# Kernel tuning notes

Measured on AMD Instinct MI355X. Metric: run time of the kernel, lower is better.

## Reference

```python
import jax, jax.numpy as jnp
import numpy as np

N = 100000          # nodes
E = 1600000         # edges (avg degree 16)
IN_F = 256          # in_features
OUT_F = 128         # out_features


def setup_inputs() -> dict:
    key = jax.random.key(0)
    k1, k2, k3, k4, k5 = jax.random.split(key, 5)
    x = jax.random.normal(k1, (N, IN_F), dtype=jnp.float32)
    edge_index = jax.random.randint(k2, (2, E), 0, N, dtype=jnp.int32)
    # xavier_uniform-style init (gain 1.414)
    def xav(k, shape):
        fan_in, fan_out = shape[0], shape[1]
        bound = 1.414 * np.sqrt(6.0 / (fan_in + fan_out))
        return jax.random.uniform(k, shape, jnp.float32, -bound, bound)
    W = xav(k3, (IN_F, OUT_F))
    a = xav(k4, (2 * OUT_F, 1))
    W_em = xav(k5, (IN_F, OUT_F))
    return {"x": x, "edge_index": edge_index, "W": W, "a": a, "W_em": W_em}


def reference(x, edge_index, W, a, W_em):
    # DisGALayer.forward_sparse, att_type=1, gnn_type='AT', eval mode (dropout off)
    src = edge_index[0]
    dst = edge_index[1]
    h = x @ W                                   # [N, OUT_F]
    # edge_e = cat(h[src], h[dst]) @ a  ==  h[src]@a_src + h[dst]@a_dst
    a_src, a_dst = a[:OUT_F], a[OUT_F:]
    edge_e = h[src] @ a_src + h[dst] @ a_dst    # [E, 1]
    edge_ob = jax.nn.sigmoid(edge_e)            # [E, 1]
    # sp_softmax: softmax of edge values grouped by row (src)
    v = jnp.exp(edge_ob - jax.lax.stop_gradient(edge_ob.max()))
    denom = jax.ops.segment_sum(v, src, num_segments=N)   # [N, 1]
    attention = v / denom[src]                  # [E, 1]
    # sp_matmul: h_prime[i] = sum_{e: src(e)=i} att_e * h_em[dst(e)]
    h_em = x @ W_em                             # [N, OUT_F]
    h_prime = jax.ops.segment_sum(attention * h_em[dst], src, num_segments=N)
    return h_prime, edge_e
```

## Files before the change

### kernel.cpp

```cpp
#include <hip/hip_runtime.h>
#include <hip/hip_bf16.h>

#define NN 100000
#define NE 1600000
#define INF 256
#define OUTF 128
#define NBK ((NN + 127) / 128)
#define CHUNK 4096
#define NBA ((NE + CHUNK - 1) / CHUNK)
#define NGRP (NN / 32)
#define SCAP 6144

typedef __attribute__((ext_vector_type(8))) short short8;
typedef __attribute__((ext_vector_type(4))) float f32x4;

static __device__ __forceinline__ short f2bf(float f) {
    __hip_bfloat16 h = __float2bfloat16(f);
    return *reinterpret_cast<short*>(&h);
}

__global__ void k_setup(const float* __restrict__ W, const float* __restrict__ a,
                        const float* __restrict__ Wem, const int* __restrict__ src,
                        float* __restrict__ wsv, float* __restrict__ wdv,
                        ushort* __restrict__ Bsw, int* __restrict__ cntA) {
    const int b = blockIdx.x, t = threadIdx.x;
    if (b == 0) {
        const float* Wr = W + (size_t)t * OUTF;
        float sa = 0.f, sb = 0.f;
        #pragma unroll 8
        for (int k = 0; k < OUTF; ++k) {
            float w = Wr[k];
            sa += w * a[k];
            sb += w * a[OUTF + k];
        }
        wsv[t] = sa;
        wdv[t] = sb;
    } else if (b <= 8) {
        const int kt = b - 1;
        for (int idx = t; idx < 4096; idx += 256) {
            const int ct = idx >> 9;
            const int lane = (idx >> 3) & 63;
            const int j = idx & 7;
            const int k = kt * 32 + (lane >> 4) * 8 + j;
            const int c = ct * 16 + (lane & 15);
            Bsw[((size_t)(kt * 8 + ct) * 64 + lane) * 8 + j] =
                (ushort)f2bf(Wem[(size_t)k * OUTF + c]);
        }
    } else {
        __shared__ int cnt[NBK];
        const int c = b - 9;
        const int e0 = c * CHUNK;
        for (int i = t; i < NBK; i += 256) cnt[i] = 0;
        __syncthreads();
        for (int i = t; i < CHUNK; i += 256) {
            const int e = e0 + i;
            if (e < NE) atomicAdd(&cnt[src[e] >> 7], 1);
        }
        __syncthreads();
        for (int i = t; i < NBK; i += 256) cntA[(size_t)c * NBK + i] = cnt[i];
    }
}

__global__ __launch_bounds__(512) void k_mmcs(
    const float* __restrict__ x, const ushort* __restrict__ Bsw,
    const float* __restrict__ wsv, const float* __restrict__ wdv,
    const int* __restrict__ cntA,
    float* __restrict__ s1, float* __restrict__ s2,
    char* __restrict__ hem8, float* __restrict__ scaleA,
    int* __restrict__ baseA, int* __restrict__ bsumB) {
    __shared__ int sm[512];
    const int b = blockIdx.x;
    const int t = threadIdx.x;
    if (b < 782) {
        const int w = t >> 6, lane = t & 63;
        const int br = b * 128 + w * 16;
        const int r0 = lane & 15, kq = lane >> 4;
        const int row = br + r0;
        const int rowc = (row < NN) ? row : NN - 1;
        const float* xp = x + (size_t)rowc * INF + kq * 8;
        const short8* bp = reinterpret_cast<const short8*>(Bsw);

        f32x4 acc[8];
        #pragma unroll
        for (int ct = 0; ct < 8; ++ct) acc[ct] = (f32x4){0.f, 0.f, 0.f, 0.f};
        float sa = 0.f, sb = 0.f;

        #pragma unroll
        for (int kt = 0; kt < 8; ++kt) {
            const float4 a0 = *reinterpret_cast<const float4*>(xp + kt * 32);
            const float4 a1 = *reinterpret_cast<const float4*>(xp + kt * 32 + 4);
            const float4 w0 = *reinterpret_cast<const float4*>(wsv + kt * 32 + kq * 8);
            const float4 w1 = *reinterpret_cast<const float4*>(wsv + kt * 32 + kq * 8 + 4);
            const float4 u0 = *reinterpret_cast<const float4*>(wdv + kt * 32 + kq * 8);
            const float4 u1 = *reinterpret_cast<const float4*>(wdv + kt * 32 + kq * 8 + 4);
            sa += a0.x * w0.x + a0.y * w0.y + a0.z * w0.z + a0.w * w0.w
                + a1.x * w1.x + a1.y * w1.y + a1.z * w1.z + a1.w * w1.w;
            sb += a0.x * u0.x + a0.y * u0.y + a0.z * u0.z + a0.w * u0.w
                + a1.x * u1.x + a1.y * u1.y + a1.z * u1.z + a1.w * u1.w;
            short8 af;
            af[0] = f2bf(a0.x); af[1] = f2bf(a0.y); af[2] = f2bf(a0.z); af[3] = f2bf(a0.w);
            af[4] = f2bf(a1.x); af[5] = f2bf(a1.y); af[6] = f2bf(a1.z); af[7] = f2bf(a1.w);
            #pragma unroll
            for (int ct = 0; ct < 8; ++ct) {
                const short8 bf = bp[(size_t)(kt * 8 + ct) * 64 + lane];
                acc[ct] = __builtin_amdgcn_mfma_f32_16x16x32_bf16(af, bf, acc[ct], 0, 0, 0);
            }
        }

        sa += __shfl_xor(sa, 16); sa += __shfl_xor(sa, 32);
        sb += __shfl_xor(sb, 16); sb += __shfl_xor(sb, 32);
        if (kq == 0 && row < NN) { s1[row] = sa; s2[row] = sb; }

        float mx[4];
        #pragma unroll
        for (int i = 0; i < 4; ++i) {
            float m = 0.f;
            #pragma unroll
            for (int ct = 0; ct < 8; ++ct) m = fmaxf(m, fabsf(acc[ct][i]));
            m = fmaxf(m, __shfl_xor(m, 1));
            m = fmaxf(m, __shfl_xor(m, 2));
            m = fmaxf(m, __shfl_xor(m, 4));
            m = fmaxf(m, __shfl_xor(m, 8));
            mx[i] = m;
        }
        #pragma unroll
        for (int i = 0; i < 4; ++i) {
            const int rr = br + kq * 4 + i;
            if (rr < NN) {
                if (r0 == 0) scaleA[rr] = mx[i];
                const float inv = (mx[i] > 0.f) ? 127.f / mx[i] : 0.f;
                #pragma unroll
                for (int ct = 0; ct < 8; ++ct) {
                    int q = (int)rintf(acc[ct][i] * inv);
                    q = (q > 127) ? 127 : ((q < -127) ? -127 : q);
                    hem8[((size_t)(ct >> 1) * NN + rr) * 32 + (ct & 1) * 16 + r0] =
                        (char)q;
                }
            }
        }
    } else {
        const int bb = b - 782;
        const int v = (t < NBA) ? cntA[(size_t)t * NBK + bb] : 0;
        sm[t] = v;
        __syncthreads();
        for (int off = 1; off < 512; off <<= 1) {
            const int add = (t >= off) ? sm[t - off] : 0;
            __syncthreads();
            sm[t] += add;
            __syncthreads();
        }
        if (t < NBA) baseA[(size_t)t * NBK + bb] = sm[t] - v;
        if (t == 511) bsumB[bb] = sm[511];
    }
}

__global__ __launch_bounds__(1024) void k_bbase(
    const int* __restrict__ bsumB, int* __restrict__ bbase,
    int* __restrict__ offs) {
    __shared__ int sm[1024];
    const int t = threadIdx.x;
    const int v = (t < NBK) ? bsumB[t] : 0;
    sm[t] = v;
    __syncthreads();
    for (int off = 1; off < 1024; off <<= 1) {
        const int add = (t >= off) ? sm[t - off] : 0;
        __syncthreads();
        sm[t] += add;
        __syncthreads();
    }
    if (t < NBK) bbase[t] = sm[t] - v;
    if (t == 0) { bbase[NBK] = NE; offs[NN] = NE; }
}

__global__ __launch_bounds__(256) void k_binA(
    const int* __restrict__ src, const int* __restrict__ dst,
    const float* __restrict__ s1, const float* __restrict__ s2,
    float* __restrict__ ee_out, const int* __restrict__ bbase,
    const int* __restrict__ baseA, int2* __restrict__ ebA) {
    __shared__ int base[NBK];
    __shared__ int cnt[NBK];
    const int t = threadIdx.x;
    const int c = blockIdx.x;
    const int e0 = c * CHUNK;
    for (int i = t; i < NBK; i += 256) {
        base[i] = bbase[i] + baseA[(size_t)c * NBK + i];
        cnt[i] = 0;
    }
    __syncthreads();
    for (int i = t; i < CHUNK; i += 256) {
        const int e = e0 + i;
        if (e < NE) {
            const int s = src[e], d = dst[e];
            const float ee = s1[s] + s2[d];
            __builtin_nontemporal_store(ee, ee_out + e);
            const float ob = 1.f / (1.f + __expf(-ee));
            const float v = __expf(ob);
            int vq = (int)((v - 1.f) * 16384.f + 0.5f);
            vq = (vq > 32767) ? 32767 : vq;
            const int bk = s >> 7;
            const int r = atomicAdd(&cnt[bk], 1);
            ebA[base[bk] + r] = make_int2((d << 7) | (s & 127), vq);
        }
    }
}

__global__ __launch_bounds__(256) void k_sortB(
    const int* __restrict__ bbase, const int2* __restrict__ ebA,
    const float* __restrict__ scaleA,
    uint* __restrict__ ebB, int* __restrict__ offs) {
    __shared__ uint rx[SCAP];
    __shared__ ushort ry[SCAP];
    __shared__ int cnt[128];
    __shared__ int sum[128];
    __shared__ int sm[128];
    __shared__ int cur[128];
    __shared__ float fsl[128];
    const int b = blockIdx.x, t = threadIdx.x;
    const int n0 = b << 7;
    const int lo = bbase[b];
    const int hi = bbase[b + 1];
    const int n = hi - lo;
    if (t < 128) { cnt[t] = 0; sum[t] = 0; }
    __syncthreads();
    for (int i = t; i < n; i += 256) {
        const int2 r = ebA[lo + i];
        if (i < SCAP) { rx[i] = (uint)r.x; ry[i] = (ushort)r.y; }
        const int sidx = r.x & 127;
        atomicAdd(&cnt[sidx], 1);
        atomicAdd(&sum[sidx], r.y);
    }
    __syncthreads();
    const int v = (t < 128) ? cnt[t] : 0;
    if (t < 128) sm[t] = v;
    __syncthreads();
    for (int off = 1; off < 128; off <<= 1) {
        int add = 0;
        if (t < 128 && t >= off) add = sm[t - off];
        __syncthreads();
        if (t < 128) sm[t] += add;
        __syncthreads();
    }
    if (t < 128) {
        const int excl = sm[t] - v;
        cur[t] = excl;
        const int node = n0 + t;
        if (node < NN) offs[node] = lo + excl;
        fsl[t] = (v > 0) ? 1.f / (float)(v * 16384 + sum[t]) : 0.f;
    }
    __syncthreads();
    for (int i = t; i < n; i += 256) {
        uint x;
        int y;
        if (i < SCAP) { x = rx[i]; y = (int)ry[i]; }
        else { const int2 r = ebA[lo + i]; x = (uint)r.x; y = r.y; }
        const int sidx = x & 127;
        const uint d = x >> 7;
        const float att = (float)(16384 + y) * fsl[sidx];
        const float w = att * scaleA[d];
        int wq = (int)(w * 1024.f + 0.5f);
        wq = (wq > 32767) ? 32767 : wq;
        const int p = atomicAdd(&cur[sidx], 1);
        ebB[lo + p] = (d << 15) | (uint)wq;
    }
}

__global__ __launch_bounds__(256) void k_aggregate(
    const uint* __restrict__ eb, const int* __restrict__ offs,
    const char* __restrict__ hem8, float* __restrict__ out0) {
    const int slice = blockIdx.x & 3;
    const int grp = blockIdx.x >> 2;
    const int t = threadIdx.x;
    const int node = grp * 32 + (t >> 3);
    const int f = t & 7;
    const char* base = hem8 + (size_t)slice * NN * 32 + f * 4;
    const int beg = offs[node];
    const int end = offs[node + 1];

    int a0 = 0, a1 = 0, a2 = 0, a3 = 0;
    int j = beg;
    for (; j + 4 <= end; j += 4) {
        const uint r0 = eb[j];
        const uint r1 = eb[j + 1];
        const uint r2 = eb[j + 2];
        const uint r3 = eb[j + 3];
        const int w0 = (int)(r0 & 0x7fffu);
        const int w1 = (int)(r1 & 0x7fffu);
        const int w2 = (int)(r2 & 0x7fffu);
        const int w3 = (int)(r3 & 0x7fffu);
        const uint u0 = *reinterpret_cast<const uint*>(base + ((size_t)(r0 >> 15)) * 32);
        const uint u1 = *reinterpret_cast<const uint*>(base + ((size_t)(r1 >> 15)) * 32);
        const uint u2 = *reinterpret_cast<const uint*>(base + ((size_t)(r2 >> 15)) * 32);
        const uint u3 = *reinterpret_cast<const uint*>(base + ((size_t)(r3 >> 15)) * 32);
        a0 += w0 * (((int)(u0 << 24)) >> 24) + w1 * (((int)(u1 << 24)) >> 24)
            + w2 * (((int)(u2 << 24)) >> 24) + w3 * (((int)(u3 << 24)) >> 24);
        a1 += w0 * (((int)(u0 << 16)) >> 24) + w1 * (((int)(u1 << 16)) >> 24)
            + w2 * (((int)(u2 << 16)) >> 24) + w3 * (((int)(u3 << 16)) >> 24);
        a2 += w0 * (((int)(u0 << 8)) >> 24) + w1 * (((int)(u1 << 8)) >> 24)
            + w2 * (((int)(u2 << 8)) >> 24) + w3 * (((int)(u3 << 8)) >> 24);
        a3 += w0 * (((int)u0) >> 24) + w1 * (((int)u1) >> 24)
            + w2 * (((int)u2) >> 24) + w3 * (((int)u3) >> 24);
    }
    for (; j < end; ++j) {
        const uint r0 = eb[j];
        const int w0 = (int)(r0 & 0x7fffu);
        const uint u0 = *reinterpret_cast<const uint*>(base + ((size_t)(r0 >> 15)) * 32);
        a0 += w0 * (((int)(u0 << 24)) >> 24);
        a1 += w0 * (((int)(u0 << 16)) >> 24);
        a2 += w0 * (((int)(u0 << 8)) >> 24);
        a3 += w0 * (((int)u0) >> 24);
    }
    const float s = 1.f / (1024.f * 127.f);
    f32x4 o = {a0 * s, a1 * s, a2 * s, a3 * s};
    *reinterpret_cast<f32x4*>(
        out0 + (size_t)node * OUTF + slice * 32 + f * 4) = o;
}

extern "C" void kernel_launch(void* const* d_in, const int* in_sizes, int n_in,
                              void* d_out, int out_size, void* d_ws, size_t ws_size,
                              hipStream_t stream) {
    const float* x   = (const float*)d_in[0];
    const int* eidx  = (const int*)d_in[1];
    const float* W   = (const float*)d_in[2];
    const float* a   = (const float*)d_in[3];
    const float* Wem = (const float*)d_in[4];

    const int* src = eidx;
    const int* dst = eidx + NE;

    float* out0 = (float*)d_out;
    float* out1 = out0 + (size_t)NN * OUTF;

    float* wsv    = (float*)d_ws;
    float* wdv    = wsv + 256;
    float* s1     = wdv + 256;
    float* s2     = s1 + NN;
    float* scaleA = s2 + NN;
    ushort* Bsw   = (ushort*)(scaleA + NN);
    int* offs     = (int*)(Bsw + 32768);
    int* bsumB    = offs + NN + 4;
    int* bbase    = bsumB + 784;
    int* cntA     = bbase + 788;
    int* baseA    = cntA + NBA * NBK;
    int2* ebA     = (int2*)(baseA + NBA * NBK);
    uint* ebB     = (uint*)(ebA + NE);
    char* hem8    = (char*)(ebB + NE);

    hipLaunchKernelGGL(k_setup, dim3(9 + NBA), dim3(256), 0, stream,
                       W, a, Wem, src, wsv, wdv, Bsw, cntA);
    hipLaunchKernelGGL(k_mmcs, dim3(782 + 782), dim3(512), 0, stream,
                       x, Bsw, wsv, wdv, cntA, s1, s2, hem8, scaleA,
                       baseA, bsumB);
    hipLaunchKernelGGL(k_bbase, dim3(1), dim3(1024), 0, stream, bsumB, bbase, offs);
    hipLaunchKernelGGL(k_binA, dim3(NBA), dim3(256), 0, stream,
                       src, dst, s1, s2, out1, bbase, baseA, ebA);
    hipLaunchKernelGGL(k_sortB, dim3(NBK), dim3(256), 0, stream,
                       bbase, ebA, scaleA, ebB, offs);
    hipLaunchKernelGGL(k_aggregate, dim3(4 * NGRP), dim3(256), 0, stream,
                       ebB, offs, hem8, out0);
}
```

Before: 156.1 us.

## Shrink mmcs blocks, prefetch x rows, and pack int8 stores via shuffles

The fused matmul/scan kernel now uses 256-thread blocks covering 64 rows each, doubling the matmul grid, and the scan half processes two elements per thread. All x loads for a row are issued up front into registers before the MFMA loop, so global memory latency overlaps. The int8 quantized output is packed across lanes with shuffles so one thread writes a 4-byte word instead of four single-byte stores. This raises register pressure and adds shuffle instructions in exchange for fewer, wider stores and more loads in flight.

```diff
diff --git a/kernel.cpp b/kernel.cpp
--- a/kernel.cpp
+++ b/kernel.cpp
@@ -10,6 +10,7 @@
 #define NBA ((NE + CHUNK - 1) / CHUNK)
 #define NGRP (NN / 32)
 #define SCAP 6144
+#define NMM 1563
 
 typedef __attribute__((ext_vector_type(8))) short short8;
 typedef __attribute__((ext_vector_type(4))) float f32x4;
@@ -61,7 +62,7 @@
     }
 }
 
-__global__ __launch_bounds__(512) void k_mmcs(
+__global__ __launch_bounds__(256) void k_mmcs(
     const float* __restrict__ x, const ushort* __restrict__ Bsw,
     const float* __restrict__ wsv, const float* __restrict__ wdv,
     const int* __restrict__ cntA,
@@ -71,15 +72,22 @@
     __shared__ int sm[512];
     const int b = blockIdx.x;
     const int t = threadIdx.x;
-    if (b < 782) {
+    if (b < NMM) {
         const int w = t >> 6, lane = t & 63;
-        const int br = b * 128 + w * 16;
+        const int br = b * 64 + w * 16;
         const int r0 = lane & 15, kq = lane >> 4;
         const int row = br + r0;
         const int rowc = (row < NN) ? row : NN - 1;
         const float* xp = x + (size_t)rowc * INF + kq * 8;
+
+        float4 xa[16];
+        #pragma unroll
+        for (int kt = 0; kt < 8; ++kt) {
+            xa[2 * kt]     = *reinterpret_cast<const float4*>(xp + kt * 32);
+            xa[2 * kt + 1] = *reinterpret_cast<const float4*>(xp + kt * 32 + 4);
+        }
+
         const short8* bp = reinterpret_cast<const short8*>(Bsw);
-
         f32x4 acc[8];
         #pragma unroll
         for (int ct = 0; ct < 8; ++ct) acc[ct] = (f32x4){0.f, 0.f, 0.f, 0.f};
@@ -87,8 +95,8 @@
 
         #pragma unroll
         for (int kt = 0; kt < 8; ++kt) {
-            const float4 a0 = *reinterpret_cast<const float4*>(xp + kt * 32);
-            const float4 a1 = *reinterpret_cast<const float4*>(xp + kt * 32 + 4);
+            const float4 a0 = xa[2 * kt];
+            const float4 a1 = xa[2 * kt + 1];
             const float4 w0 = *reinterpret_cast<const float4*>(wsv + kt * 32 + kq * 8);
             const float4 w1 = *reinterpret_cast<const float4*>(wsv + kt * 32 + kq * 8 + 4);
             const float4 u0 = *reinterpret_cast<const float4*>(wdv + kt * 32 + kq * 8);
@@ -126,31 +134,41 @@
         #pragma unroll
         for (int i = 0; i < 4; ++i) {
             const int rr = br + kq * 4 + i;
-            if (rr < NN) {
-                if (r0 == 0) scaleA[rr] = mx[i];
-                const float inv = (mx[i] > 0.f) ? 127.f / mx[i] : 0.f;
-                #pragma unroll
-                for (int ct = 0; ct < 8; ++ct) {
-                    int q = (int)rintf(acc[ct][i] * inv);
-                    q = (q > 127) ? 127 : ((q < -127) ? -127 : q);
-                    hem8[((size_t)(ct >> 1) * NN + rr) * 32 + (ct & 1) * 16 + r0] =
-                        (char)q;
+            const float inv = (mx[i] > 0.f) ? 127.f / mx[i] : 0.f;
+            if (r0 == 0 && rr < NN) scaleA[rr] = mx[i];
+            #pragma unroll
+            for (int ct = 0; ct < 8; ++ct) {
+                int q = (int)rintf(acc[ct][i] * inv);
+                q = (q > 127) ? 127 : ((q < -127) ? -127 : q);
+                uint p = (uint)(q & 255);
+                p |= ((uint)__shfl_xor((int)p, 1) & 255u) << 8;
+                uint word = p | ((uint)__shfl_xor((int)p, 2) << 16);
+                if ((r0 & 3) == 0 && rr < NN) {
+                    *reinterpret_cast<uint*>(
+                        hem8 + ((size_t)(ct >> 1) * NN + rr) * 32
+                             + (ct & 1) * 16 + r0) = word;
                 }
             }
         }
     } else {
-        const int bb = b - 782;
-        const int v = (t < NBA) ? cntA[(size_t)t * NBK + bb] : 0;
-        sm[t] = v;
+        const int bb = b - NMM;
+        const int v0 = (t < NBA) ? cntA[(size_t)t * NBK + bb] : 0;
+        const int t2 = t + 256;
+        const int v1 = (t2 < NBA) ? cntA[(size_t)t2 * NBK + bb] : 0;
+        sm[t] = v0;
+        sm[t2] = v1;
         __syncthreads();
         for (int off = 1; off < 512; off <<= 1) {
-            const int add = (t >= off) ? sm[t - off] : 0;
+            const int a0 = (t >= off) ? sm[t - off] : 0;
+            const int a1 = (t2 >= off) ? sm[t2 - off] : 0;
             __syncthreads();
-            sm[t] += add;
+            sm[t] += a0;
+            sm[t2] += a1;
             __syncthreads();
         }
-        if (t < NBA) baseA[(size_t)t * NBK + bb] = sm[t] - v;
-        if (t == 511) bsumB[bb] = sm[511];
+        if (t < NBA) baseA[(size_t)t * NBK + bb] = sm[t] - v0;
+        if (t2 < NBA) baseA[(size_t)t2 * NBK + bb] = sm[t2] - v1;
+        if (t == 255) bsumB[bb] = sm[511];
     }
 }
 
@@ -347,7 +365,7 @@
 
     hipLaunchKernelGGL(k_setup, dim3(9 + NBA), dim3(256), 0, stream,
                        W, a, Wem, src, wsv, wdv, Bsw, cntA);
-    hipLaunchKernelGGL(k_mmcs, dim3(782 + 782), dim3(512), 0, stream,
+    hipLaunchKernelGGL(k_mmcs, dim3(NMM + NBK), dim3(256), 0, stream,
                        x, Bsw, wsv, wdv, cntA, s1, s2, hem8, scaleA,
                        baseA, bsumB);
     hipLaunchKernelGGL(k_bbase, dim3(1), dim3(1024), 0, stream, bsumB, bbase, offs);
```

New measurement: 154.6 us. Within noise of the previous version (-0.9%).
